# Kernel tuning notes

Measured on AMD Instinct MI355X. Metric: run time of the kernel, lower is better.

Reference implementation:

```python
import jax, jax.numpy as jnp
import numpy as np

PRE_NMS_LIMIT = 6000
PROPOSAL_COUNT = 2000
NMS_THRESHOLD = 0.7
BBOX_STD = np.array([0.1, 0.1, 0.2, 0.2], dtype=np.float32)  # RPN_BBOX_STD_DEV


def setup_inputs() -> dict:
    key = jax.random.key(0)
    k1, k2, k3, k4 = jax.random.split(key, 4)
    B, N = 2, 262144
    # rpn_probs: softmax over (bg, fg) so column 1 is a valid fg probability
    rpn_probs = jax.nn.softmax(jax.random.normal(k1, (B, N, 2), dtype=jnp.float32), axis=-1)
    rpn_bbox = jax.random.normal(k2, (B, N, 4), dtype=jnp.float32)
    # anchors in normalized coords with y1<y2, x1<x2
    yx = jax.random.uniform(k3, (B, N, 2), dtype=jnp.float32) * 0.9
    hw = jax.random.uniform(k4, (B, N, 2), dtype=jnp.float32) * 0.1 + 0.005
    anchors = jnp.concatenate([yx, yx + hw], axis=-1)
    return {"rpn_probs": rpn_probs, "rpn_bbox": rpn_bbox, "anchors": anchors}


def _nms_single(boxes, scores):
    """Greedy NMS on score-sorted boxes [K,4]; returns [PROPOSAL_COUNT,4] padded."""
    K = boxes.shape[0]
    y1, x1, y2, x2 = boxes[:, 0], boxes[:, 1], boxes[:, 2], boxes[:, 3]
    areas = (y2 - y1) * (x2 - x1)
    iy1 = jnp.maximum(y1[:, None], y1[None, :])
    ix1 = jnp.maximum(x1[:, None], x1[None, :])
    iy2 = jnp.minimum(y2[:, None], y2[None, :])
    ix2 = jnp.minimum(x2[:, None], x2[None, :])
    inter = jnp.maximum(iy2 - iy1, 0.0) * jnp.maximum(ix2 - ix1, 0.0)
    union = areas[:, None] + areas[None, :] - inter
    iou = jnp.where(union > 0.0, inter / union, 0.0)  # [K, K]
    idxs = jnp.arange(K)

    def body(suppressed, xs):
        row, i = xs
        keep_i = jnp.logical_not(suppressed[i])
        suppressed = suppressed | (keep_i & (row > NMS_THRESHOLD) & (idxs > i))
        return suppressed, keep_i

    _, keep = jax.lax.scan(body, jnp.zeros((K,), bool), (iou, idxs))
    # gather kept boxes in score order, truncate/pad to PROPOSAL_COUNT
    rank = jnp.cumsum(keep) - 1
    valid = keep & (rank < PROPOSAL_COUNT)
    dest = jnp.where(valid, rank, PROPOSAL_COUNT)  # overflow bucket at index P
    out = jnp.zeros((PROPOSAL_COUNT + 1, 4), boxes.dtype)
    out = out.at[dest].set(jnp.where(valid[:, None], boxes, 0.0))
    return out[:PROPOSAL_COUNT]


def reference(rpn_probs, rpn_bbox, anchors):
    scores = rpn_probs[:, :, 1]  # fg prob [B, N]
    deltas = rpn_bbox * jnp.asarray(BBOX_STD).reshape(1, 1, 4)
    k = min(PRE_NMS_LIMIT, anchors.shape[1])
    top_scores, ix = jax.lax.top_k(scores, k)  # sorted desc, [B, K]
    gather = lambda a: jnp.take_along_axis(a, ix[..., None], axis=1)
    d = gather(deltas)       # [B, K, 4]
    a = gather(anchors)      # [B, K, 4]
    # apply_box_deltas_graph (vectorized over batch)
    h = a[..., 2] - a[..., 0]
    w = a[..., 3] - a[..., 1]
    cy = a[..., 0] + 0.5 * h + d[..., 0] * h
    cx = a[..., 1] + 0.5 * w + d[..., 1] * w
    h = h * jnp.exp(d[..., 2])
    w = w * jnp.exp(d[..., 3])
    y1 = cy - 0.5 * h
    x1 = cx - 0.5 * w
    boxes = jnp.stack([y1, x1, y1 + h, x1 + w], axis=-1)
    # clip to window (0, 0, 1, 1)
    boxes = jnp.clip(boxes, 0.0, 1.0)
    proposals = jax.vmap(_nms_single)(boxes, top_scores)  # [B, P, 4]
    return proposals
```

## Files before the change

### kernel.cpp

```cpp
#include <hip/hip_runtime.h>
#include <stdint.h>

typedef unsigned long long u64;

#define NB 2
#define N_ANCHORS 262144
#define LOG2N 18
#define PRE_NMS 6000
#define PROPOSALS 2000
#define NCHUNK 94
#define CAND_CAP 8192
#define HBINS 16384
#define HB_BLOCKS_PER_B 64
#define HB_CHUNK (N_ANCHORS / HB_BLOCKS_PER_B)
#define CB_BLOCKS_PER_B 64
#define CB_CHUNK (N_ANCHORS / CB_BLOCKS_PER_B)
#define CBUF 512
#define WINDOW 2048
#define EDGE_CAP 65536
#define EDGE_LDS 16384

#define OFF_HIST 0
#define OFF_BCNT (NB*HBINS*4)
#define OFF_SCAL (2*NB*HBINS*4)
#define OFF_CAND (OFF_SCAL + 256)
#define OFF_SUFF (OFF_CAND + NB*CAND_CAP*8)
#define OFF_BOXES (OFF_SUFF + NB*HBINS*4)
#define OFF_EDGES (OFF_BOXES + NB*PRE_NMS*16)
#define OFF_HROWS (OFF_EDGES + NB*EDGE_CAP*4)


__global__ __launch_bounds__(256) void hist_kernel(const float4* __restrict__ probs4,
                                                   unsigned* __restrict__ hrows) {
    __shared__ unsigned lh[HBINS];
    int t = threadIdx.x;
    for (int j = t; j < HBINS; j += 256) lh[j] = 0u;
    __syncthreads();
    int b   = blockIdx.x / HB_BLOCKS_PER_B;
    int blk = blockIdx.x % HB_BLOCKS_PER_B;
    const float4* p = probs4 + ((size_t)b * N_ANCHORS + (size_t)blk * HB_CHUNK) / 2;
    #pragma unroll 4
    for (int k = 0; k < HB_CHUNK / 512; ++k) {
        float4 v = p[k * 256 + t];
        unsigned bin0 = __float_as_uint(v.y) >> 16;
        unsigned bin1 = __float_as_uint(v.w) >> 16;
        if (bin0 > HBINS - 1) bin0 = HBINS - 1;
        if (bin1 > HBINS - 1) bin1 = HBINS - 1;
        atomicAdd(&lh[bin0], 1u);
        atomicAdd(&lh[bin1], 1u);
    }
    __syncthreads();
    unsigned* row = hrows + (size_t)(b * HB_BLOCKS_PER_B + blk) * HBINS;
    for (int j = t; j < HBINS; j += 256) row[j] = lh[j];
}

__global__ __launch_bounds__(256) void hist_reduce(const unsigned* __restrict__ hrows,
                                                   unsigned* __restrict__ hist) {
    int b   = blockIdx.x / (HBINS / 256);
    int blk = blockIdx.x % (HBINS / 256);
    int bin = blk * 256 + threadIdx.x;
    const unsigned* base = hrows + (size_t)b * HB_BLOCKS_PER_B * HBINS + bin;
    unsigned s = 0;
    #pragma unroll 8
    for (int r = 0; r < HB_BLOCKS_PER_B; ++r) s += base[(size_t)r * HBINS];
    hist[(size_t)b * HBINS + bin] = s;
}

__global__ __launch_bounds__(1024) void scan_sel(const unsigned* __restrict__ hist,
                                                 int* __restrict__ scal,
                                                 unsigned* __restrict__ suff,
                                                 unsigned* __restrict__ binCnt) {
    int b = blockIdx.x;
    const unsigned* h = hist + (size_t)b * HBINS;
    unsigned* sf = suff + (size_t)b * HBINS;
    unsigned* bc = binCnt + (size_t)b * HBINS;
    int t = threadIdx.x;
    for (int j = t; j < HBINS; j += 1024) bc[j] = 0u;
    if (t == 0) scal[b * 8 + 5] = 0;
    unsigned base = t * 16;
    unsigned hl[16];
    unsigned s = 0;
    #pragma unroll
    for (int j = 0; j < 16; ++j) { hl[j] = h[base + j]; s += hl[j]; }
    __shared__ unsigned buf[1024];
    buf[t] = s;
    __syncthreads();
    for (int off = 1; off < 1024; off <<= 1) {
        unsigned v = buf[t] + ((t + off < 1024) ? buf[t + off] : 0u);
        __syncthreads();
        buf[t] = v;
        __syncthreads();
    }
    unsigned run = (t < 1023) ? buf[t + 1] : 0u;
    #pragma unroll
    for (int j = 15; j >= 0; --j) {
        sf[base + j] = run;
        run += hl[j];
    }
    unsigned sufInc = buf[t];
    unsigned sufBefore = sufInc - s;
    if (sufBefore < PRE_NMS && sufInc >= PRE_NMS) {
        unsigned r2 = sufBefore;
        unsigned T = 0, totC = 0;
        for (int j = 15; j >= 0; --j) {
            if (r2 + hl[j] >= PRE_NMS) { T = base + j; totC = r2 + hl[j]; break; }
            r2 += hl[j];
        }
        if (totC > CAND_CAP) totC = CAND_CAP;
        scal[b * 8 + 2] = (int)(T << 16);
        scal[b * 8 + 6] = (int)totC;
    }
}

__global__ __launch_bounds__(256) void compact(const float4* __restrict__ probs4,
                                               const int* __restrict__ scal,
                                               const unsigned* __restrict__ suff,
                                               unsigned* __restrict__ binCnt,
                                               u64* __restrict__ cand) {
    __shared__ unsigned lcnt[WINDOW];
    __shared__ u64 keyBuf[CBUF];
    __shared__ unsigned slotBuf[CBUF];
    __shared__ int nc;
    int t = threadIdx.x;
    int b   = blockIdx.x / CB_BLOCKS_PER_B;
    int blk = blockIdx.x % CB_BLOCKS_PER_B;
    for (int j = t; j < WINDOW; j += 256) lcnt[j] = 0u;
    if (t == 0) nc = 0;
    __syncthreads();
    unsigned kthr = (unsigned)scal[b * 8 + 2];
    unsigned T = kthr >> 16;
    const unsigned* sfB = suff + (size_t)b * HBINS;
    unsigned* bcB = binCnt + (size_t)b * HBINS;
    u64* candB = cand + (size_t)b * CAND_CAP;
    size_t anchor0 = (size_t)blk * CB_CHUNK;
    const float4* p = probs4 + ((size_t)b * N_ANCHORS + anchor0) / 2;
    #pragma unroll 2
    for (int k = 0; k < CB_CHUNK / 512; ++k) {
        float4 v = p[k * 256 + t];
        unsigned n0 = (unsigned)(anchor0 + ((size_t)(k * 256 + t)) * 2);
        unsigned keys[2] = { __float_as_uint(v.y), __float_as_uint(v.w) };
        #pragma unroll
        for (int e = 0; e < 2; ++e) {
            unsigned key = keys[e];
            if (key >= kthr) {
                unsigned bin = key >> 16;
                unsigned rel = bin - T;
                u64 k64 = ((u64)key << 32) | (u64)(~(n0 + e));
                int idx;
                if (rel < WINDOW && (idx = atomicAdd(&nc, 1)) < CBUF) {
                    unsigned slot = atomicAdd(&lcnt[rel], 1u);
                    keyBuf[idx] = k64;
                    slotBuf[idx] = slot;
                } else {
                    unsigned gs = atomicAdd(&bcB[bin], 1u);
                    unsigned pos = sfB[bin] + gs;
                    if (pos < CAND_CAP) candB[pos] = k64;
                }
            }
        }
    }
    __syncthreads();
    for (int j = t; j < WINDOW; j += 256) {
        unsigned c = lcnt[j];
        if (c) lcnt[j] = atomicAdd(&bcB[T + j], c);
    }
    __syncthreads();
    int tot = nc < CBUF ? nc : CBUF;
    for (int k = t; k < tot; k += 256) {
        u64 k64 = keyBuf[k];
        unsigned bin = (unsigned)(k64 >> 48);
        unsigned pos = sfB[bin] + lcnt[bin - T] + slotBuf[k];
        if (pos < CAND_CAP) candB[pos] = k64;
    }
}

__global__ __launch_bounds__(256) void refine_decode(const u64* __restrict__ cand,
                                                     const int* __restrict__ scal,
                                                     const unsigned* __restrict__ suff,
                                                     const unsigned* __restrict__ binCnt,
                                                     const float* __restrict__ anchors,
                                                     const float* __restrict__ bbox,
                                                     float4* __restrict__ boxes) {
    int b = blockIdx.y;
    int wave = threadIdx.x >> 6;
    int lane = threadIdx.x & 63;
    int p = blockIdx.x * 4 + wave;
    if (p >= scal[b * 8 + 6]) return;
    u64 my = cand[(size_t)b * CAND_CAP + p];
    unsigned bin = (unsigned)(my >> 48);
    unsigned s = suff[(size_t)b * HBINS + bin];
    if (s >= PRE_NMS) return;
    unsigned c = binCnt[(size_t)b * HBINS + bin];
    if (s + c > CAND_CAP) c = CAND_CAP - s;
    const u64* seg = cand + (size_t)b * CAND_CAP + s;
    int cnt = 0;
    for (unsigned q = lane; q < c; q += 64)
        cnt += (seg[q] > my) ? 1 : 0;
    #pragma unroll
    for (int off = 32; off; off >>= 1) cnt += __shfl_down(cnt, off, 64);
    int rank = (int)s + __shfl(cnt, 0, 64);
    if (rank < PRE_NMS && lane == 0) {
        int n = (int)(~(unsigned)(my & 0xFFFFFFFFull));
        const float4* anch4 = (const float4*)anchors + (size_t)b * N_ANCHORS;
        const float4* bb4   = (const float4*)bbox    + (size_t)b * N_ANCHORS;
        float4 a  = anch4[n];
        float4 dd = bb4[n];
        float d0 = dd.x * 0.1f, d1 = dd.y * 0.1f;
        float d2 = dd.z * 0.2f, d3 = dd.w * 0.2f;
        float h = a.z - a.x, w = a.w - a.y;
        float cy = a.x + 0.5f * h + d0 * h;
        float cx = a.y + 0.5f * w + d1 * w;
        h = h * expf(d2);
        w = w * expf(d3);
        float y1 = cy - 0.5f * h, x1 = cx - 0.5f * w;
        float y2 = y1 + h,        x2 = x1 + w;
        y1 = fminf(fmaxf(y1, 0.f), 1.f);
        x1 = fminf(fmaxf(x1, 0.f), 1.f);
        y2 = fminf(fmaxf(y2, 0.f), 1.f);
        x2 = fminf(fmaxf(x2, 0.f), 1.f);
        boxes[(size_t)b * PRE_NMS + rank] = make_float4(y1, x1, y2, x2);
    }
}

__global__ __launch_bounds__(256) void iou_edges(const float4* __restrict__ boxes,
                                                 int* __restrict__ scal,
                                                 unsigned* __restrict__ edges) {
    int c  = blockIdx.x;
    int rb = blockIdx.y;
    int b  = blockIdx.z;
    int rowBase = rb * 256;
    if (rowBase >= (c + 1) * 64) return;
    const float4* bx = boxes + (size_t)b * PRE_NMS;
    __shared__ float4 cb[64];
    __shared__ float  ca[64];
    int t = threadIdx.x;
    if (t < 64) {
        int col = c * 64 + t;
        float4 v = (col < PRE_NMS) ? bx[col] : make_float4(2.f, 2.f, 2.f, 2.f);
        cb[t] = v;
        ca[t] = (v.z - v.x) * (v.w - v.y);
    }
    __syncthreads();
    int i = rowBase + t;
    if (i >= PRE_NMS) return;
    int rel = i - c * 64;
    u64 maskGT = (rel < 0) ? ~0ull : ((rel >= 63) ? 0ull : ~((2ull << rel) - 1ull));
    if (!maskGT) return;
    float4 bi = bx[i];
    float ai = (bi.z - bi.x) * (bi.w - bi.y);
    u64 m = 0ull;
    #pragma unroll
    for (int j = 0; j < 64; ++j) {
        float4 bj = cb[j];
        float iy1 = fmaxf(bi.x, bj.x);
        float ix1 = fmaxf(bi.y, bj.y);
        float iy2 = fminf(bi.z, bj.z);
        float ix2 = fminf(bi.w, bj.w);
        float inter = fmaxf(iy2 - iy1, 0.f) * fmaxf(ix2 - ix1, 0.f);
        float uni = ai + ca[j] - inter;
        if (inter > 0.7f * uni) m |= (1ull << j);
    }
    m &= maskGT;
    while (m) {
        int j = __ffsll((long long)m) - 1;
        m &= m - 1;
        int col = c * 64 + j;
        int pos = atomicAdd(&scal[b * 8 + 5], 1);
        if (pos < EDGE_CAP)
            edges[(size_t)b * EDGE_CAP + pos] = ((unsigned)col << 16) | (unsigned)i;
    }
}

__global__ __launch_bounds__(256) void nms_fix(const unsigned* __restrict__ edges,
                                               const int* __restrict__ scal,
                                               const float4* __restrict__ boxes,
                                               float4* __restrict__ out) {
    int b = blockIdx.x;
    int t = threadIdx.x;
    int E = scal[b * 8 + 5];
    if (E > EDGE_CAP) E = EDGE_CAP;
    __shared__ u64 S[NCHUNK];
    __shared__ u64 Snew[NCHUNK];
    __shared__ unsigned eL[EDGE_LDS];
    __shared__ int changed;
    __shared__ int pref[NCHUNK];
    __shared__ int totalKept;
    const unsigned* eg = edges + (size_t)b * EDGE_CAP;
    bool staged = (E <= EDGE_LDS);
    if (staged) for (int k = t; k < E; k += 256) eL[k] = eg[k];
    for (int w = t; w < NCHUNK; w += 256) S[w] = 0ull;
    __syncthreads();
    if (E > 0) {
        for (int it = 0; it < PRE_NMS + 1; ++it) {
            for (int w = t; w < NCHUNK; w += 256) Snew[w] = 0ull;
            if (t == 0) changed = 0;
            __syncthreads();
            for (int k = t; k < E; k += 256) {
                unsigned e = staged ? eL[k] : eg[k];
                int i = (int)(e & 0xFFFFu), j = (int)(e >> 16);
                if (!((S[i >> 6] >> (i & 63)) & 1ull))
                    atomicOr(&Snew[j >> 6], 1ull << (j & 63));
            }
            __syncthreads();
            int ch = 0;
            for (int w = t; w < NCHUNK; w += 256) {
                if (Snew[w] != S[w]) { ch = 1; S[w] = Snew[w]; }
            }
            if (ch) changed = 1;
            __syncthreads();
            if (!changed) break;
        }
    }
    for (int w = t; w < NCHUNK; w += 256) {
        u64 valid = (w < NCHUNK - 1) ? ~0ull : ((1ull << (PRE_NMS - (NCHUNK - 1) * 64)) - 1ull);
        Snew[w] = (~S[w]) & valid;
    }
    __syncthreads();
    if (t == 0) {
        int run = 0;
        for (int w = 0; w < NCHUNK; ++w) { pref[w] = run; run += __popcll(Snew[w]); }
        totalKept = (run < PROPOSALS) ? run : PROPOSALS;
    }
    __syncthreads();
    const float4* bx = boxes + (size_t)b * PRE_NMS;
    float4* ob = out + (size_t)b * PROPOSALS;
    if (t < NCHUNK) {
        u64 k = Snew[t];
        int pos = pref[t];
        while (k && pos < PROPOSALS) {
            int l = __ffsll((long long)k) - 1;
            k &= k - 1;
            ob[pos++] = bx[t * 64 + l];
        }
    }
    int tk = totalKept;
    for (int q = tk + t; q < PROPOSALS; q += 256)
        ob[q] = make_float4(0.f, 0.f, 0.f, 0.f);
}

extern "C" void kernel_launch(void* const* d_in, const int* in_sizes, int n_in,
                              void* d_out, int out_size, void* d_ws, size_t ws_size,
                              hipStream_t stream) {
    (void)in_sizes; (void)n_in; (void)out_size; (void)ws_size;
    const float4* probs4 = (const float4*)d_in[0];
    const float* bbox    = (const float*)d_in[1];
    const float* anchors = (const float*)d_in[2];
    char* ws = (char*)d_ws;
    unsigned* hist   = (unsigned*)(ws + OFF_HIST);
    unsigned* binCnt = (unsigned*)(ws + OFF_BCNT);
    int* scal        = (int*)(ws + OFF_SCAL);
    u64* cand        = (u64*)(ws + OFF_CAND);
    unsigned* suff   = (unsigned*)(ws + OFF_SUFF);
    float4* boxes    = (float4*)(ws + OFF_BOXES);
    unsigned* edges  = (unsigned*)(ws + OFF_EDGES);
    unsigned* hrows  = (unsigned*)(ws + OFF_HROWS);

    hist_kernel<<<NB * HB_BLOCKS_PER_B, 256, 0, stream>>>(probs4, hrows);
    hist_reduce<<<NB * (HBINS / 256), 256, 0, stream>>>(hrows, hist);
    scan_sel<<<NB, 1024, 0, stream>>>(hist, scal, suff, binCnt);
    compact<<<NB * CB_BLOCKS_PER_B, 256, 0, stream>>>(probs4, scal, suff, binCnt, cand);
    refine_decode<<<dim3(CAND_CAP / 4, NB), 256, 0, stream>>>(cand, scal, suff, binCnt,
                                                              anchors, bbox, boxes);
    dim3 gIou(NCHUNK, (PRE_NMS + 255) / 256, NB);
    iou_edges<<<gIou, 256, 0, stream>>>(boxes, scal, edges);
    nms_fix<<<NB, 256, 0, stream>>>(edges, scal, boxes, (float4*)d_out);
}
```

Baseline: 76.04 us.

## Fuse histogram reduce with scan and IoU with NMS via last-block pattern

```diff
diff --git a/kernel.cpp b/kernel.cpp
--- a/kernel.cpp
+++ b/kernel.cpp
@@ -5,20 +5,21 @@
 
 #define NB 2
 #define N_ANCHORS 262144
-#define LOG2N 18
 #define PRE_NMS 6000
 #define PROPOSALS 2000
 #define NCHUNK 94
 #define CAND_CAP 8192
 #define HBINS 16384
-#define HB_BLOCKS_PER_B 64
+#define HB_BLOCKS_PER_B 32
 #define HB_CHUNK (N_ANCHORS / HB_BLOCKS_PER_B)
+#define HR_BLOCKS_PER_B 16
 #define CB_BLOCKS_PER_B 64
 #define CB_CHUNK (N_ANCHORS / CB_BLOCKS_PER_B)
 #define CBUF 512
 #define WINDOW 2048
 #define EDGE_CAP 65536
-#define EDGE_LDS 16384
+#define EDGE_LDS 4096
+#define IOU_BLOCKS_PER_B (NCHUNK * ((PRE_NMS + 255) / 256))
 
 #define OFF_HIST 0
 #define OFF_BCNT (NB*HBINS*4)
@@ -30,18 +31,20 @@
 #define OFF_HROWS (OFF_EDGES + NB*EDGE_CAP*4)
 
 
-__global__ __launch_bounds__(256) void hist_kernel(const float4* __restrict__ probs4,
-                                                   unsigned* __restrict__ hrows) {
+__global__ __launch_bounds__(1024) void hist_kernel(const float4* __restrict__ probs4,
+                                                    unsigned* __restrict__ hrows,
+                                                    int* __restrict__ scal) {
     __shared__ unsigned lh[HBINS];
     int t = threadIdx.x;
-    for (int j = t; j < HBINS; j += 256) lh[j] = 0u;
-    __syncthreads();
+    for (int j = t; j < HBINS; j += 1024) lh[j] = 0u;
     int b   = blockIdx.x / HB_BLOCKS_PER_B;
     int blk = blockIdx.x % HB_BLOCKS_PER_B;
+    if (blk == 0 && t == 0) { scal[b * 8 + 0] = 0; scal[b * 8 + 7] = 0; }
+    __syncthreads();
     const float4* p = probs4 + ((size_t)b * N_ANCHORS + (size_t)blk * HB_CHUNK) / 2;
-    #pragma unroll 4
-    for (int k = 0; k < HB_CHUNK / 512; ++k) {
-        float4 v = p[k * 256 + t];
+    #pragma unroll
+    for (int k = 0; k < HB_CHUNK / 2048; ++k) {
+        float4 v = p[k * 1024 + t];
         unsigned bin0 = __float_as_uint(v.y) >> 16;
         unsigned bin1 = __float_as_uint(v.w) >> 16;
         if (bin0 > HBINS - 1) bin0 = HBINS - 1;
@@ -51,37 +54,42 @@
     }
     __syncthreads();
     unsigned* row = hrows + (size_t)(b * HB_BLOCKS_PER_B + blk) * HBINS;
-    for (int j = t; j < HBINS; j += 256) row[j] = lh[j];
-}
-
-__global__ __launch_bounds__(256) void hist_reduce(const unsigned* __restrict__ hrows,
-                                                   unsigned* __restrict__ hist) {
-    int b   = blockIdx.x / (HBINS / 256);
-    int blk = blockIdx.x % (HBINS / 256);
-    int bin = blk * 256 + threadIdx.x;
+    for (int j = t; j < HBINS; j += 1024) row[j] = lh[j];
+}
+
+__global__ __launch_bounds__(1024) void reduce_scan(const unsigned* __restrict__ hrows,
+                                                    unsigned* __restrict__ hist,
+                                                    int* __restrict__ scal,
+                                                    unsigned* __restrict__ suff,
+                                                    unsigned* __restrict__ binCnt) {
+    int t = threadIdx.x;
+    int b   = blockIdx.x / HR_BLOCKS_PER_B;
+    int blk = blockIdx.x % HR_BLOCKS_PER_B;
+    int bin = blk * 1024 + t;
     const unsigned* base = hrows + (size_t)b * HB_BLOCKS_PER_B * HBINS + bin;
-    unsigned s = 0;
-    #pragma unroll 8
-    for (int r = 0; r < HB_BLOCKS_PER_B; ++r) s += base[(size_t)r * HBINS];
-    hist[(size_t)b * HBINS + bin] = s;
-}
-
-__global__ __launch_bounds__(1024) void scan_sel(const unsigned* __restrict__ hist,
-                                                 int* __restrict__ scal,
-                                                 unsigned* __restrict__ suff,
-                                                 unsigned* __restrict__ binCnt) {
-    int b = blockIdx.x;
+    unsigned s0 = 0;
+    #pragma unroll
+    for (int r = 0; r < HB_BLOCKS_PER_B; ++r) s0 += base[(size_t)r * HBINS];
+    hist[(size_t)b * HBINS + bin] = s0;
+    __shared__ int amLast;
+    __syncthreads();
+    if (t == 0) {
+        __threadfence();
+        amLast = (atomicAdd(&scal[b * 8 + 0], 1) == HR_BLOCKS_PER_B - 1);
+    }
+    __syncthreads();
+    if (!amLast) return;
+    __threadfence();
     const unsigned* h = hist + (size_t)b * HBINS;
     unsigned* sf = suff + (size_t)b * HBINS;
     unsigned* bc = binCnt + (size_t)b * HBINS;
-    int t = threadIdx.x;
     for (int j = t; j < HBINS; j += 1024) bc[j] = 0u;
     if (t == 0) scal[b * 8 + 5] = 0;
-    unsigned base = t * 16;
+    unsigned bbase = t * 16;
     unsigned hl[16];
     unsigned s = 0;
     #pragma unroll
-    for (int j = 0; j < 16; ++j) { hl[j] = h[base + j]; s += hl[j]; }
+    for (int j = 0; j < 16; ++j) { hl[j] = h[bbase + j]; s += hl[j]; }
     __shared__ unsigned buf[1024];
     buf[t] = s;
     __syncthreads();
@@ -94,7 +102,7 @@
     unsigned run = (t < 1023) ? buf[t + 1] : 0u;
     #pragma unroll
     for (int j = 15; j >= 0; --j) {
-        sf[base + j] = run;
+        sf[bbase + j] = run;
         run += hl[j];
     }
     unsigned sufInc = buf[t];
@@ -103,7 +111,7 @@
         unsigned r2 = sufBefore;
         unsigned T = 0, totC = 0;
         for (int j = 15; j >= 0; --j) {
-            if (r2 + hl[j] >= PRE_NMS) { T = base + j; totC = r2 + hl[j]; break; }
+            if (r2 + hl[j] >= PRE_NMS) { T = bbase + j; totC = r2 + hl[j]; break; }
             r2 += hl[j];
         }
         if (totC > CAND_CAP) totC = CAND_CAP;
@@ -222,61 +230,67 @@
     }
 }
 
-__global__ __launch_bounds__(256) void iou_edges(const float4* __restrict__ boxes,
-                                                 int* __restrict__ scal,
-                                                 unsigned* __restrict__ edges) {
+__global__ __launch_bounds__(256) void iou_nms(const float4* __restrict__ boxes,
+                                               int* __restrict__ scal,
+                                               unsigned* __restrict__ edges,
+                                               float4* __restrict__ out) {
     int c  = blockIdx.x;
     int rb = blockIdx.y;
     int b  = blockIdx.z;
-    int rowBase = rb * 256;
-    if (rowBase >= (c + 1) * 64) return;
+    int t = threadIdx.x;
     const float4* bx = boxes + (size_t)b * PRE_NMS;
     __shared__ float4 cb[64];
     __shared__ float  ca[64];
-    int t = threadIdx.x;
-    if (t < 64) {
-        int col = c * 64 + t;
-        float4 v = (col < PRE_NMS) ? bx[col] : make_float4(2.f, 2.f, 2.f, 2.f);
-        cb[t] = v;
-        ca[t] = (v.z - v.x) * (v.w - v.y);
-    }
-    __syncthreads();
-    int i = rowBase + t;
-    if (i >= PRE_NMS) return;
-    int rel = i - c * 64;
-    u64 maskGT = (rel < 0) ? ~0ull : ((rel >= 63) ? 0ull : ~((2ull << rel) - 1ull));
-    if (!maskGT) return;
-    float4 bi = bx[i];
-    float ai = (bi.z - bi.x) * (bi.w - bi.y);
-    u64 m = 0ull;
-    #pragma unroll
-    for (int j = 0; j < 64; ++j) {
-        float4 bj = cb[j];
-        float iy1 = fmaxf(bi.x, bj.x);
-        float ix1 = fmaxf(bi.y, bj.y);
-        float iy2 = fminf(bi.z, bj.z);
-        float ix2 = fminf(bi.w, bj.w);
-        float inter = fmaxf(iy2 - iy1, 0.f) * fmaxf(ix2 - ix1, 0.f);
-        float uni = ai + ca[j] - inter;
-        if (inter > 0.7f * uni) m |= (1ull << j);
-    }
-    m &= maskGT;
-    while (m) {
-        int j = __ffsll((long long)m) - 1;
-        m &= m - 1;
-        int col = c * 64 + j;
-        int pos = atomicAdd(&scal[b * 8 + 5], 1);
-        if (pos < EDGE_CAP)
-            edges[(size_t)b * EDGE_CAP + pos] = ((unsigned)col << 16) | (unsigned)i;
-    }
-}
-
-__global__ __launch_bounds__(256) void nms_fix(const unsigned* __restrict__ edges,
-                                               const int* __restrict__ scal,
-                                               const float4* __restrict__ boxes,
-                                               float4* __restrict__ out) {
-    int b = blockIdx.x;
-    int t = threadIdx.x;
+    int rowBase = rb * 256;
+    bool active = rowBase < (c + 1) * 64;
+    if (active) {
+        if (t < 64) {
+            int col = c * 64 + t;
+            float4 v = (col < PRE_NMS) ? bx[col] : make_float4(2.f, 2.f, 2.f, 2.f);
+            cb[t] = v;
+            ca[t] = (v.z - v.x) * (v.w - v.y);
+        }
+        __syncthreads();
+        int i = rowBase + t;
+        if (i < PRE_NMS) {
+            int rel = i - c * 64;
+            u64 maskGT = (rel < 0) ? ~0ull : ((rel >= 63) ? 0ull : ~((2ull << rel) - 1ull));
+            if (maskGT) {
+                float4 bi = bx[i];
+                float ai = (bi.z - bi.x) * (bi.w - bi.y);
+                u64 m = 0ull;
+                #pragma unroll
+                for (int j = 0; j < 64; ++j) {
+                    float4 bj = cb[j];
+                    float iy1 = fmaxf(bi.x, bj.x);
+                    float ix1 = fmaxf(bi.y, bj.y);
+                    float iy2 = fminf(bi.z, bj.z);
+                    float ix2 = fminf(bi.w, bj.w);
+                    float inter = fmaxf(iy2 - iy1, 0.f) * fmaxf(ix2 - ix1, 0.f);
+                    float uni = ai + ca[j] - inter;
+                    if (inter > 0.7f * uni) m |= (1ull << j);
+                }
+                m &= maskGT;
+                while (m) {
+                    int j = __ffsll((long long)m) - 1;
+                    m &= m - 1;
+                    int col = c * 64 + j;
+                    int pos = atomicAdd(&scal[b * 8 + 5], 1);
+                    if (pos < EDGE_CAP)
+                        edges[(size_t)b * EDGE_CAP + pos] = ((unsigned)col << 16) | (unsigned)i;
+                }
+            }
+        }
+    }
+    __shared__ int amLast;
+    __syncthreads();
+    if (t == 0) {
+        __threadfence();
+        amLast = (atomicAdd(&scal[b * 8 + 7], 1) == IOU_BLOCKS_PER_B - 1);
+    }
+    __syncthreads();
+    if (!amLast) return;
+    __threadfence();
     int E = scal[b * 8 + 5];
     if (E > EDGE_CAP) E = EDGE_CAP;
     __shared__ u64 S[NCHUNK];
@@ -322,7 +336,6 @@
         totalKept = (run < PROPOSALS) ? run : PROPOSALS;
     }
     __syncthreads();
-    const float4* bx = boxes + (size_t)b * PRE_NMS;
     float4* ob = out + (size_t)b * PROPOSALS;
     if (t < NCHUNK) {
         u64 k = Snew[t];
@@ -355,13 +368,11 @@
     unsigned* edges  = (unsigned*)(ws + OFF_EDGES);
     unsigned* hrows  = (unsigned*)(ws + OFF_HROWS);
 
-    hist_kernel<<<NB * HB_BLOCKS_PER_B, 256, 0, stream>>>(probs4, hrows);
-    hist_reduce<<<NB * (HBINS / 256), 256, 0, stream>>>(hrows, hist);
-    scan_sel<<<NB, 1024, 0, stream>>>(hist, scal, suff, binCnt);
+    hist_kernel<<<NB * HB_BLOCKS_PER_B, 1024, 0, stream>>>(probs4, hrows, scal);
+    reduce_scan<<<NB * HR_BLOCKS_PER_B, 1024, 0, stream>>>(hrows, hist, scal, suff, binCnt);
     compact<<<NB * CB_BLOCKS_PER_B, 256, 0, stream>>>(probs4, scal, suff, binCnt, cand);
     refine_decode<<<dim3(CAND_CAP / 4, NB), 256, 0, stream>>>(cand, scal, suff, binCnt,
                                                               anchors, bbox, boxes);
     dim3 gIou(NCHUNK, (PRE_NMS + 255) / 256, NB);
-    iou_edges<<<gIou, 256, 0, stream>>>(boxes, scal, edges);
-    nms_fix<<<NB, 256, 0, stream>>>(edges, scal, boxes, (float4*)d_out);
-}
+    iou_nms<<<gIou, 256, 0, stream>>>(boxes, scal, edges, (float4*)d_out);
+}
```

After: 135.1 us. 77.7% more time.
